# Optimization experiments

Measured on AMD Instinct MI355X. Metric: run time of the kernel, lower is better.

The kernel has to match this reference:

```python
import jax, jax.numpy as jnp
import numpy as np

N = 100000   # nodes
E = 1600000  # edges
F = 64       # node_features == latent_channels
H = 128      # hidden_channels
G = 256      # graphs
L = 2        # n_layers


def setup_inputs() -> dict:
    key = jax.random.key(0)
    ks = jax.random.split(key, 20)
    x = jax.random.normal(ks[0], (N, F), dtype=jnp.float32)
    u = jax.random.normal(ks[1], (G, 2), dtype=jnp.float32)
    edge_index = jax.random.randint(ks[2], (2, E), 0, N, dtype=jnp.int32)
    # evenly assign nodes to graphs (sorted segment ids, no empty segments)
    batch = (jnp.arange(N, dtype=jnp.int32) * G // N).astype(jnp.int32)
    s = 0.05
    # per-layer edge-MLP params, stacked over layers: in = 2F-2 = 126
    W1 = jax.random.normal(ks[3], (L, 2 * F - 2, H), dtype=jnp.float32) * s
    b1 = jnp.zeros((L, H), dtype=jnp.float32)
    W2 = jax.random.normal(ks[4], (L, H, H), dtype=jnp.float32) * s
    b2 = jnp.zeros((L, H), dtype=jnp.float32)
    W3 = jax.random.normal(ks[5], (L, H, F), dtype=jnp.float32) * s
    b3 = jnp.zeros((L, F), dtype=jnp.float32)
    # readout head: in = 3*F + 2 = 194
    LW1 = jax.random.normal(ks[6], (3 * F + 2, F), dtype=jnp.float32) * s
    Lb1 = jnp.zeros((F,), dtype=jnp.float32)
    LW2 = jax.random.normal(ks[7], (F, F), dtype=jnp.float32) * s
    Lb2 = jnp.zeros((F,), dtype=jnp.float32)
    LW3 = jax.random.normal(ks[8], (F, 2), dtype=jnp.float32) * s
    Lb3 = jnp.zeros((2,), dtype=jnp.float32)
    return dict(x=x, u=u, edge_index=edge_index, batch=batch,
                W1=W1, b1=b1, W2=W2, b2=b2, W3=W3, b3=b3,
                LW1=LW1, Lb1=Lb1, LW2=LW2, Lb2=Lb2, LW3=LW3, Lb3=Lb3)


def _edge_layer(x, src, dst, W1, b1, W2, b2, W3, b3):
    xi = x[dst]            # target nodes (x_i), [E, F]
    xj = x[src]            # source nodes (x_j), [E, F]
    d = xj[:, :3] - xi[:, :3]
    dist2 = jnp.sum(d * d, axis=-1, keepdims=True)  # [E, 1]
    m_in = jnp.concatenate([xi, xj[:, 3:], dist2], axis=-1)  # [E, 2F-2]
    h = jax.nn.silu(m_in @ W1 + b1)
    h = jax.nn.silu(h @ W2 + b2)
    m = jax.nn.silu(h @ W3 + b3)                    # [E, F]
    return jax.ops.segment_sum(m, dst, num_segments=N)  # aggr='sum'


def reference(x, u, edge_index, batch, W1, b1, W2, b2, W3, b3,
              LW1, Lb1, LW2, Lb2, LW3, Lb3):
    src, dst = edge_index[0], edge_index[1]
    for l in range(L):
        x = _edge_layer(x, src, dst, W1[l], b1[l], W2[l], b2[l], W3[l], b3[l])
    addp = jax.ops.segment_sum(x, batch, num_segments=G)
    cnt = jax.ops.segment_sum(jnp.ones((N, 1), x.dtype), batch, num_segments=G)
    meanp = addp / jnp.maximum(cnt, 1.0)
    maxp = jax.ops.segment_max(x, batch, num_segments=G)
    pooled = jnp.concatenate([addp, meanp, maxp, u], axis=1)  # [G, 3F+2]
    h = jax.nn.silu(pooled @ LW1 + Lb1)
    h = jax.nn.silu(h @ LW2 + Lb2)
    return h @ LW3 + Lb3  # [G, 2]
```

## Files before the change

### kernel.cpp

```cpp
#include <hip/hip_runtime.h>
#include <hip/hip_bf16.h>

typedef _Float16 f16;
typedef _Float16 f16x8 __attribute__((ext_vector_type(8)));
typedef float    f32x4 __attribute__((ext_vector_type(4)));
typedef float    f32x8 __attribute__((ext_vector_type(8)));

__device__ __forceinline__ float silu_f(float x) {
    return x * __builtin_amdgcn_rcpf(1.0f + __expf(-x));
}

__device__ __forceinline__ f16 exp2h(f16 x) {
    short r, xs = __builtin_bit_cast(short, x);
    asm("v_exp_f16 %0, %1" : "=v"(r) : "v"(xs));
    return __builtin_bit_cast(f16, r);
}
__device__ __forceinline__ f16 rcph(f16 x) {
    short r, xs = __builtin_bit_cast(short, x);
    asm("v_rcp_f16 %0, %1" : "=v"(r) : "v"(xs));
    return __builtin_bit_cast(f16, r);
}
__device__ __forceinline__ f16x8 silu_h8(f16x8 x) {
    f16x8 t = x * (f16)(-1.442695040f);
    f16x8 e;
#pragma unroll
    for (int j = 0; j < 8; j++) e[j] = exp2h(t[j]);
    f16x8 d = e + (f16)1.0f;
    f16x8 r;
#pragma unroll
    for (int j = 0; j < 8; j++) r[j] = rcph(d[j]);
    return x * r;
}

__device__ __forceinline__ void load_lds16(const f16* g, f16* l) {
    __builtin_amdgcn_global_load_lds(
        (const __attribute__((address_space(1))) void*)g,
        (__attribute__((address_space(3))) void*)l, 16, 0, 0);
}

__global__ void prep_kernel(const float* __restrict__ W1, const float* __restrict__ W2,
                            const float* __restrict__ W3, f16* __restrict__ B1T,
                            f16* __restrict__ W2T, f16* __restrict__ W3T,
                            f16* __restrict__ w1c, int L, int total) {
    int idx = blockIdx.x * 256 + threadIdx.x;
    if (idx >= total) return;
    const int per = 16384 + 16384 + 8192 + 128;
    int l = idx / per, r = idx % per;
    const float* W1l = W1 + (size_t)l * 126 * 128;
    if (r < 16384) {
        int c = r >> 6, k = r & 63;
        float v;
        if (c < 128) v = W1l[k * 128 + c];
        else v = (k >= 3) ? W1l[(64 + k - 3) * 128 + (c - 128)] : 0.0f;
        B1T[(size_t)l * 16384 + r] = (f16)v;
    } else if (r < 32768) {
        int q = r - 16384, n = q >> 7, k = q & 127;
        W2T[(size_t)l * 16384 + q] = (f16)W2[(size_t)l * 16384 + k * 128 + n];
    } else if (r < 40960) {
        int q = r - 32768, n = q >> 7, k = q & 127;
        W3T[(size_t)l * 8192 + q] = (f16)W3[(size_t)l * 8192 + k * 64 + n];
    } else {
        int c = r - 40960;
        w1c[l * 128 + c] = (f16)W1l[125 * 128 + c];
    }
}

__global__ void hist_kernel(const int* __restrict__ ei, int* __restrict__ deg, int E) {
    int i = blockIdx.x * 256 + threadIdx.x;
    if (i < E) atomicAdd(&deg[ei[E + i]], 1);
}

__global__ void scan_part(const int* __restrict__ deg, int* __restrict__ bsum, int N) {
    __shared__ int red[256];
    int t = threadIdx.x;
    int i = blockIdx.x * 256 + t;
    red[t] = (i < N) ? deg[i] : 0;
    __syncthreads();
    for (int s = 128; s > 0; s >>= 1) {
        if (t < s) red[t] += red[t + s];
        __syncthreads();
    }
    if (t == 0) bsum[blockIdx.x] = red[0];
}

__global__ void scan_mid(const int* __restrict__ bsum, int* __restrict__ boff, int nb) {
    __shared__ int sm[512];
    int t = threadIdx.x;
    int v = (t < nb) ? bsum[t] : 0;
    sm[t] = v;
    __syncthreads();
    for (int off = 1; off < 512; off <<= 1) {
        int a = (t >= off) ? sm[t - off] : 0;
        __syncthreads();
        sm[t] += a;
        __syncthreads();
    }
    if (t < nb) boff[t] = sm[t] - v;
}

__global__ void scan_final(const int* __restrict__ deg, const int* __restrict__ boff,
                           int* __restrict__ row_start, int N) {
    __shared__ int sm[256];
    int t = threadIdx.x;
    int i = blockIdx.x * 256 + t;
    int v = (i < N) ? deg[i] : 0;
    sm[t] = v;
    __syncthreads();
    for (int off = 1; off < 256; off <<= 1) {
        int a = (t >= off) ? sm[t - off] : 0;
        __syncthreads();
        sm[t] += a;
        __syncthreads();
    }
    if (i < N) row_start[i] = boff[blockIdx.x] + sm[t] - v;
}

__global__ void scatter_kernel(const int* __restrict__ ei, const int* __restrict__ row_start,
                               int* __restrict__ cursor, int2* __restrict__ sd, int E) {
    int i = blockIdx.x * 256 + threadIdx.x;
    if (i < E) {
        int d = ei[E + i];
        int p = row_start[d] + atomicAdd(&cursor[d], 1);
        sd[p] = make_int2(ei[i], d);
    }
}

__global__ __launch_bounds__(256, 3) void node_kernel(
    const float* __restrict__ x, const f16* __restrict__ B1T,
    const float* __restrict__ b1, f16* __restrict__ PQ,
    float4* __restrict__ C, int N, int ntiles) {
    __shared__ f16 b1t[256 * 72];
    const int tid = threadIdx.x;
    const int w = tid >> 6, lane = tid & 63, lm = lane & 15, kg = lane >> 4;

    for (int i = tid; i < 256 * 64; i += 256)
        b1t[(i >> 6) * 72 + (i & 63)] = B1T[i];
    __syncthreads();

    for (int tile = blockIdx.x; tile < ntiles; tile += gridDim.x) {
        const int base = tile * 64;
        int ar = base + w * 16 + lm;
        if (ar >= N) ar = N - 1;

        f16x8 afrag[2];
#pragma unroll
        for (int ks = 0; ks < 2; ks++) {
            f32x8 v = *(const f32x8*)(x + (size_t)ar * 64 + ks * 32 + kg * 8);
            f16x8 h;
#pragma unroll
            for (int j = 0; j < 8; j++) h[j] = (f16)v[j];
            afrag[ks] = h;
        }

        f32x4 acc[16];
#pragma unroll
        for (int nb = 0; nb < 16; nb++) acc[nb] = (f32x4){0.f, 0.f, 0.f, 0.f};
#pragma unroll
        for (int ks = 0; ks < 2; ks++)
#pragma unroll
            for (int nb = 0; nb < 16; nb++) {
                f16x8 b = *(const f16x8*)&b1t[(nb * 16 + lm) * 72 + ks * 32 + kg * 8];
                acc[nb] = __builtin_amdgcn_mfma_f32_16x16x32_f16(afrag[ks], b, acc[nb], 0, 0, 0);
            }

#pragma unroll
        for (int nb = 0; nb < 16; nb++) {
            int col = nb * 16 + lm;
            float bias = (col < 128) ? b1[col] : 0.0f;
#pragma unroll
            for (int reg = 0; reg < 4; reg++) {
                int orow = base + w * 16 + kg * 4 + reg;
                if (orow < N) PQ[(size_t)orow * 256 + col] = (f16)(acc[nb][reg] + bias);
            }
        }
        if (tid < 64) {
            int n = base + tid;
            if (n < N) {
                const float* xr = x + (size_t)n * 64;
                C[n] = make_float4(xr[0], xr[1], xr[2], 0.0f);
            }
        }
    }
}

__global__ __launch_bounds__(256, 3) void edge_kernel(
    const f16* __restrict__ PQ, const float4* __restrict__ C,
    const int2* __restrict__ sd,
    const f16* __restrict__ W2T, const f16* __restrict__ W3T,
    const f16* __restrict__ w1c, const float* __restrict__ b2,
    const float* __restrict__ b3, float* __restrict__ xout,
    int E, int wtiles) {
    __shared__ f16 w2t[128 * 128];
    __shared__ f16 stage[4 * 2048];
    __shared__ f16 tb[4 * 576];

    const int tid = threadIdx.x;
    const int w = tid >> 6, lane = tid & 63, lm = lane & 15, kg = lane >> 4;
    const int e4 = lane >> 2, c4 = lane & 3;

    for (int i = tid; i < 128 * 128; i += 256) {
        int n = i >> 7, k = i & 127;
        w2t[n * 128 + (((k >> 3) ^ (n & 15)) << 3) + (k & 7)] = W2T[i];
    }

    f16x8 wvh[4];
#pragma unroll
    for (int ks = 0; ks < 4; ks++) wvh[ks] = *(const f16x8*)(w1c + ks * 32 + kg * 8);
    float bias2[8], bias3[4];
#pragma unroll
    for (int nb = 0; nb < 8; nb++) bias2[nb] = b2[nb * 16 + lm];
#pragma unroll
    for (int nb = 0; nb < 4; nb++) bias3[nb] = b3[nb * 16 + lm];
    __syncthreads();

    f16* sw = stage + w * 2048;
    f16* tq = tb + w * 576;
    const int nwaves = gridDim.x * 4;
    const int r0 = kg * 4;
    const int l1i = (lane + 16) & 63, l2i = (lane + 32) & 63, l3i = (lane + 48) & 63;

    int t = blockIdx.x * 4 + w;
    if (t >= wtiles) return;
    int e0 = t * 16 + lm;
    int erc = min(e0, E - 1);
    int2 sd0 = sd[erc];
    int scl = sd0.x, dcl = sd0.y;
    int dsen_cur = (e0 < E) ? dcl : -1;
    {
        int se = __shfl(scl, e4);
        const f16* gq = PQ + (size_t)se * 256 + 128 + c4 * 8;
#pragma unroll
        for (int j = 0; j < 4; j++) load_lds16(gq + j * 32, sw + j * 512 + lane * 8);
    }
    f16x8 pv[4];
    {
        const f16* gp = PQ + (size_t)dcl * 256 + kg * 8;
#pragma unroll
        for (int ks = 0; ks < 4; ks++) pv[ks] = *(const f16x8*)(gp + ks * 32);
    }
    int e1 = (t + nwaves) * 16 + lm;
    int erc1 = min(max(e1, 0), E - 1);
    int2 sdn = sd[erc1];
    int s_nx = sdn.x, d_nx = sdn.y;
    int e_nx_ok = (e1 < E) ? 1 : 0;
    float4 cs = C[scl], cd = C[dcl];

    f32x4 acc2p[4];
#pragma unroll
    for (int nb2 = 0; nb2 < 4; nb2++) acc2p[nb2] = (f32x4){0.f, 0.f, 0.f, 0.f};
    int dsen_prev = -1;

    while (true) {
        const int tn = t + nwaves;

        asm volatile("s_waitcnt vmcnt(0)" ::: "memory");

        float dx = cs.x - cd.x, dy = cs.y - cd.y, dz = cs.z - cd.z;
        float dist2 = dx * dx + dy * dy + dz * dz;
        f16 d2h = (f16)dist2;

        f16x8 afrag[4];
#pragma unroll
        for (int ks = 0; ks < 4; ks++) {
            f16x8 q = *(const f16x8*)&sw[ks * 512 + lm * 32 + kg * 8];
            f16x8 xv = pv[ks] + q + d2h * wvh[ks];
            afrag[ks] = silu_h8(xv);
        }

        f32x4 acc1[8];
#pragma unroll
        for (int nb = 0; nb < 8; nb++) acc1[nb] = (f32x4){0.f, 0.f, 0.f, 0.f};
#pragma unroll
        for (int ks = 0; ks < 4; ks++)
#pragma unroll
            for (int nb = 0; nb < 8; nb++) {
                int n = nb * 16 + lm;
                f16x8 b = *(const f16x8*)&w2t[n * 128 + (((ks * 4 + kg) ^ (n & 15)) << 3)];
                acc1[nb] = __builtin_amdgcn_mfma_f32_16x16x32_f16(afrag[ks], b, acc1[nb], 0, 0, 0);
            }

        {
            const int dr0 = __shfl(dsen_prev, r0);
            const int dr1 = __shfl(dsen_prev, r0 + 1);
            const int dr2 = __shfl(dsen_prev, r0 + 2);
            const int dr3 = __shfl(dsen_prev, r0 + 3);
            int prevv = __shfl(dsen_prev, (r0 - 1) & 63);
            if (kg == 0) prevv = -1234567;

            const bool e01 = dr0 == dr1, e12 = dr1 == dr2, e23 = dr2 == dr3;
            const bool c01 = e01, c02 = e01 && e12, c03 = c02 && e23;
            const bool c12 = e12, c13 = e12 && e23;
            const int fullI = c03 ? 1 : 0;

            const int tgt = dr3;
            const int dr0_1 = __shfl(dr0, l1i), fu1 = __shfl(fullI, l1i);
            const int dr0_2 = __shfl(dr0, l2i), fu2 = __shfl(fullI, l2i);
            const int dr0_3 = __shfl(dr0, l3i);
            const bool take1 = (kg <= 2) && (dr0_1 == tgt);
            const bool take2 = take1 && fu1 && (kg <= 1) && (dr0_2 == tgt);
            const bool take3 = take2 && fu2 && (kg == 0) && (dr0_3 == tgt);

            const bool h0 = (dr0 != prevv) && (dr0 >= 0);
            const bool h1f = (!e01) && (dr1 >= 0);
            const bool h2f = (!e12) && (dr2 >= 0);
            const bool h3f = (!e23) && (dr3 >= 0);

            float t0v[4], t1v[4], t2v[4], t3v[4];
#pragma unroll
            for (int nb2 = 0; nb2 < 4; nb2++) {
                const float bias = bias3[nb2];
                const float v0 = silu_f(acc2p[nb2][0] + bias);
                const float v1 = silu_f(acc2p[nb2][1] + bias);
                const float v2 = silu_f(acc2p[nb2][2] + bias);
                const float v3 = silu_f(acc2p[nb2][3] + bias);
                float lead = v0 + (c01 ? v1 : 0.f) + (c02 ? v2 : 0.f) + (c03 ? v3 : 0.f);
                float ext = 0.f;
                const float le1 = __shfl(lead, l1i);
                const float le2 = __shfl(lead, l2i);
                const float le3 = __shfl(lead, l3i);
                if (take1) ext += le1;
                if (take2) ext += le2;
                if (take3) ext += le3;
                t0v[nb2] = lead + (c03 ? ext : 0.f);
                t1v[nb2] = v1 + (c12 ? v2 : 0.f) + (c13 ? (v3 + ext) : 0.f);
                t2v[nb2] = v2 + (e23 ? (v3 + ext) : 0.f);
                t3v[nb2] = v3 + ext;
            }
            if (h0) {
                float* p = xout + (size_t)dr0 * 64 + lm;
#pragma unroll
                for (int nb2 = 0; nb2 < 4; nb2++) atomicAdd(p + nb2 * 16, t0v[nb2]);
            }
            if (h1f) {
                float* p = xout + (size_t)dr1 * 64 + lm;
#pragma unroll
                for (int nb2 = 0; nb2 < 4; nb2++) atomicAdd(p + nb2 * 16, t1v[nb2]);
            }
            if (h2f) {
                float* p = xout + (size_t)dr2 * 64 + lm;
#pragma unroll
                for (int nb2 = 0; nb2 < 4; nb2++) atomicAdd(p + nb2 * 16, t2v[nb2]);
            }
            if (h3f) {
                float* p = xout + (size_t)dr3 * 64 + lm;
#pragma unroll
                for (int nb2 = 0; nb2 < 4; nb2++) atomicAdd(p + nb2 * 16, t3v[nb2]);
            }
        }

        int dsen_nx = e_nx_ok ? d_nx : -1;
        if (tn < wtiles) {
            int se = __shfl(s_nx, e4);
            const f16* gq = PQ + (size_t)se * 256 + 128 + c4 * 8;
#pragma unroll
            for (int j = 0; j < 4; j++) load_lds16(gq + j * 32, sw + j * 512 + lane * 8);
        }

        f16x8 pv2[4];
        {
            const f16* gp2 = PQ + (size_t)d_nx * 256 + kg * 8;
#pragma unroll
            for (int ks = 0; ks < 4; ks++) pv2[ks] = *(const f16x8*)(gp2 + ks * 32);
        }
        int e2 = (tn + nwaves) * 16 + lm;
        int erc2 = min(max(e2, 0), E - 1);
        int2 sd2 = sd[erc2];
        int e_nx2_ok = (e2 < E) ? 1 : 0;
        float4 cs2 = C[s_nx], cd2 = C[d_nx];

        f32x4 acc2[4];
#pragma unroll
        for (int nb2 = 0; nb2 < 4; nb2++) acc2[nb2] = (f32x4){0.f, 0.f, 0.f, 0.f};
#pragma unroll
        for (int kq = 0; kq < 4; kq++) {
#pragma unroll
            for (int nn = 0; nn < 2; nn++) {
                int nb = kq * 2 + nn;
#pragma unroll
                for (int reg = 0; reg < 4; reg++)
                    tq[(kg * 4 + reg) * 36 + nn * 16 + lm] =
                        (f16)silu_f(acc1[nb][reg] + bias2[nb]);
            }
            f16x8 a2 = *(const f16x8*)&tq[lm * 36 + kg * 8];
#pragma unroll
            for (int nb2 = 0; nb2 < 4; nb2++) {
                f16x8 b = *(const f16x8*)(W3T + (size_t)(nb2 * 16 + lm) * 128 +
                                          kq * 32 + kg * 8);
                acc2[nb2] = __builtin_amdgcn_mfma_f32_16x16x32_f16(a2, b, acc2[nb2], 0, 0, 0);
            }
        }

#pragma unroll
        for (int nb2 = 0; nb2 < 4; nb2++) acc2p[nb2] = acc2[nb2];
#pragma unroll
        for (int ks = 0; ks < 4; ks++) pv[ks] = pv2[ks];
        dsen_prev = dsen_cur;
        dsen_cur = dsen_nx;
        s_nx = sd2.x; d_nx = sd2.y; e_nx_ok = e_nx2_ok;
        cs = cs2; cd = cd2;
        t = tn;
        if (t >= wtiles) break;
    }

    {
        const int dr0 = __shfl(dsen_prev, r0);
        const int dr1 = __shfl(dsen_prev, r0 + 1);
        const int dr2 = __shfl(dsen_prev, r0 + 2);
        const int dr3 = __shfl(dsen_prev, r0 + 3);
        int prevv = __shfl(dsen_prev, (r0 - 1) & 63);
        if (kg == 0) prevv = -1234567;

        const bool e01 = dr0 == dr1, e12 = dr1 == dr2, e23 = dr2 == dr3;
        const bool c01 = e01, c02 = e01 && e12, c03 = c02 && e23;
        const bool c12 = e12, c13 = e12 && e23;
        const int fullI = c03 ? 1 : 0;

        const int tgt = dr3;
        const int dr0_1 = __shfl(dr0, l1i), fu1 = __shfl(fullI, l1i);
        const int dr0_2 = __shfl(dr0, l2i), fu2 = __shfl(fullI, l2i);
        const int dr0_3 = __shfl(dr0, l3i);
        const bool take1 = (kg <= 2) && (dr0_1 == tgt);
        const bool take2 = take1 && fu1 && (kg <= 1) && (dr0_2 == tgt);
        const bool take3 = take2 && fu2 && (kg == 0) && (dr0_3 == tgt);

        const bool h0 = (dr0 != prevv) && (dr0 >= 0);
        const bool h1f = (!e01) && (dr1 >= 0);
        const bool h2f = (!e12) && (dr2 >= 0);
        const bool h3f = (!e23) && (dr3 >= 0);

        float t0v[4], t1v[4], t2v[4], t3v[4];
#pragma unroll
        for (int nb2 = 0; nb2 < 4; nb2++) {
            const float bias = bias3[nb2];
            const float v0 = silu_f(acc2p[nb2][0] + bias);
            const float v1 = silu_f(acc2p[nb2][1] + bias);
            const float v2 = silu_f(acc2p[nb2][2] + bias);
            const float v3 = silu_f(acc2p[nb2][3] + bias);
            float lead = v0 + (c01 ? v1 : 0.f) + (c02 ? v2 : 0.f) + (c03 ? v3 : 0.f);
            float ext = 0.f;
            const float le1 = __shfl(lead, l1i);
            const float le2 = __shfl(lead, l2i);
            const float le3 = __shfl(lead, l3i);
            if (take1) ext += le1;
            if (take2) ext += le2;
            if (take3) ext += le3;
            t0v[nb2] = lead + (c03 ? ext : 0.f);
            t1v[nb2] = v1 + (c12 ? v2 : 0.f) + (c13 ? (v3 + ext) : 0.f);
            t2v[nb2] = v2 + (e23 ? (v3 + ext) : 0.f);
            t3v[nb2] = v3 + ext;
        }
        if (h0) {
            float* p = xout + (size_t)dr0 * 64 + lm;
#pragma unroll
            for (int nb2 = 0; nb2 < 4; nb2++) atomicAdd(p + nb2 * 16, t0v[nb2]);
        }
        if (h1f) {
            float* p = xout + (size_t)dr1 * 64 + lm;
#pragma unroll
            for (int nb2 = 0; nb2 < 4; nb2++) atomicAdd(p + nb2 * 16, t1v[nb2]);
        }
        if (h2f) {
            float* p = xout + (size_t)dr2 * 64 + lm;
#pragma unroll
            for (int nb2 = 0; nb2 < 4; nb2++) atomicAdd(p + nb2 * 16, t2v[nb2]);
        }
        if (h3f) {
            float* p = xout + (size_t)dr3 * 64 + lm;
#pragma unroll
            for (int nb2 = 0; nb2 < 4; nb2++) atomicAdd(p + nb2 * 16, t3v[nb2]);
        }
    }
    asm volatile("s_waitcnt vmcnt(0)" ::: "memory");
}

__global__ void pool_head_kernel(const float* __restrict__ xf, const float* __restrict__ u,
                                 const float* __restrict__ LW1, const float* __restrict__ Lb1,
                                 const float* __restrict__ LW2, const float* __restrict__ Lb2,
                                 const float* __restrict__ LW3, const float* __restrict__ Lb3,
                                 float* __restrict__ out, int N, int G) {
    int g = blockIdx.x;
    int t = threadIdx.x;
    int ch = t & 63, sub = t >> 6;
    long long n0 = ((long long)g * N + G - 1) / G;
    long long n1 = ((long long)(g + 1) * N + G - 1) / G;
    float sm = 0.f, mx = -3.0e38f;
    for (long long n = n0 + sub; n < n1; n += 4) {
        float v = xf[n * 64 + ch];
        sm += v;
        mx = fmaxf(mx, v);
    }
    __shared__ float ssum[256], smax[256];
    __shared__ float pl[194];
    __shared__ float hl[64];
    ssum[t] = sm;
    smax[t] = mx;
    __syncthreads();
    if (sub == 0) {
        float a = ssum[ch] + ssum[64 + ch] + ssum[128 + ch] + ssum[192 + ch];
        float m = fmaxf(fmaxf(smax[ch], smax[64 + ch]), fmaxf(smax[128 + ch], smax[192 + ch]));
        float cnt = (float)(n1 - n0);
        pl[ch] = a;
        pl[64 + ch] = a / fmaxf(cnt, 1.f);
        pl[128 + ch] = m;
    }
    if (t == 0) {
        pl[192] = u[g * 2];
        pl[193] = u[g * 2 + 1];
    }
    __syncthreads();
    float a = 0.f;
    if (t < 64) {
        a = Lb1[t];
        for (int k = 0; k < 194; k++) a += pl[k] * LW1[k * 64 + t];
        a = a / (1.0f + __expf(-a));
        hl[t] = a;
    }
    __syncthreads();
    float b = 0.f;
    if (t < 64) {
        b = Lb2[t];
        for (int k = 0; k < 64; k++) b += hl[k] * LW2[k * 64 + t];
        b = b / (1.0f + __expf(-b));
    }
    __syncthreads();
    if (t < 64) hl[t] = b;
    __syncthreads();
    if (t < 2) {
        float c = Lb3[t];
        for (int k = 0; k < 64; k++) c += hl[k] * LW3[k * 2 + t];
        out[g * 2 + t] = c;
    }
}

extern "C" void kernel_launch(void* const* d_in, const int* in_sizes, int n_in,
                              void* d_out, int out_size, void* d_ws, size_t ws_size,
                              hipStream_t stream) {
    const float* x   = (const float*)d_in[0];
    const float* u   = (const float*)d_in[1];
    const int*   ei  = (const int*)d_in[2];
    const float* W1  = (const float*)d_in[4];
    const float* b1  = (const float*)d_in[5];
    const float* W2  = (const float*)d_in[6];
    const float* b2  = (const float*)d_in[7];
    const float* W3  = (const float*)d_in[8];
    const float* b3  = (const float*)d_in[9];
    const float* LW1 = (const float*)d_in[10];
    const float* Lb1 = (const float*)d_in[11];
    const float* LW2 = (const float*)d_in[12];
    const float* Lb2 = (const float*)d_in[13];
    const float* LW3 = (const float*)d_in[14];
    const float* Lb3 = (const float*)d_in[15];

    const int N = in_sizes[0] / 64;
    const int G = in_sizes[1] / 2;
    const int E = in_sizes[2] / 2;
    const int L = in_sizes[4] / (126 * 128);

    char* ws = (char*)d_ws;
    size_t off = 0;
    auto alloc = [&](size_t bytes) -> char* {
        char* p = ws + off;
        off += (bytes + 511) & ~(size_t)511;
        return p;
    };
    f16*    PQ     = (f16*)alloc((size_t)N * 256 * 2);
    float4* C      = (float4*)alloc((size_t)N * 16);
    float*  x1     = (float*)alloc((size_t)N * 64 * 4);
    float*  x2     = (float*)alloc((size_t)N * 64 * 4);
    int2*   sd     = (int2*)alloc((size_t)E * 8);
    int*    deg    = (int*)alloc((size_t)N * 4);
    int*    rowst  = (int*)alloc((size_t)N * 4);
    int*    cursor = (int*)alloc((size_t)N * 4);
    int*    bsum   = (int*)alloc(4096);
    int*    boff   = (int*)alloc(4096);
    f16*    B1T    = (f16*)alloc((size_t)L * 256 * 64 * 2);
    f16*    W2T    = (f16*)alloc((size_t)L * 128 * 128 * 2);
    f16*    W3T    = (f16*)alloc((size_t)L * 64 * 128 * 2);
    f16*    w1c    = (f16*)alloc((size_t)L * 128 * 2);
    (void)ws_size;
    (void)n_in;
    (void)out_size;

    hipMemsetAsync(deg, 0, (size_t)N * 4, stream);
    hipMemsetAsync(cursor, 0, (size_t)N * 4, stream);
    hipMemsetAsync(x1, 0, (size_t)N * 64 * 4, stream);
    hipMemsetAsync(x2, 0, (size_t)N * 64 * 4, stream);

    {
        int total = L * (16384 + 16384 + 8192 + 128);
        prep_kernel<<<(total + 255) / 256, 256, 0, stream>>>(W1, W2, W3, B1T, W2T, W3T, w1c, L, total);
    }
    hist_kernel<<<(E + 255) / 256, 256, 0, stream>>>(ei, deg, E);
    int NB = (N + 255) / 256;
    scan_part<<<NB, 256, 0, stream>>>(deg, bsum, N);
    scan_mid<<<1, 512, 0, stream>>>(bsum, boff, NB);
    scan_final<<<NB, 256, 0, stream>>>(deg, boff, rowst, N);
    scatter_kernel<<<(E + 255) / 256, 256, 0, stream>>>(ei, rowst, cursor, sd, E);

    const float* xcur = x;
    const int wtiles = (E + 15) / 16;
    const int ntiles_node = (N + 63) / 64;
    for (int l = 0; l < L; l++) {
        node_kernel<<<768, 256, 0, stream>>>(xcur, B1T + (size_t)l * 16384, b1 + l * 128,
                                             PQ, C, N, ntiles_node);
        float* xo = (l & 1) ? x2 : x1;
        edge_kernel<<<768, 256, 0, stream>>>(PQ, C, sd,
                                             W2T + (size_t)l * 16384, W3T + (size_t)l * 8192,
                                             w1c + l * 128, b2 + l * 128, b3 + l * 64,
                                             xo, E, wtiles);
        xcur = xo;
    }
    pool_head_kernel<<<G, 256, 0, stream>>>(xcur, u, LW1, Lb1, LW2, Lb2, LW3, Lb3,
                                            (float*)d_out, N, G);
}
```

Baseline: 914.0 us.

## Load source rows into registers, drop LDS staging, raise occupancy to four blocks

```diff
diff --git a/kernel.cpp b/kernel.cpp
--- a/kernel.cpp
+++ b/kernel.cpp
@@ -30,12 +30,6 @@
 #pragma unroll
     for (int j = 0; j < 8; j++) r[j] = rcph(d[j]);
     return x * r;
-}
-
-__device__ __forceinline__ void load_lds16(const f16* g, f16* l) {
-    __builtin_amdgcn_global_load_lds(
-        (const __attribute__((address_space(1))) void*)g,
-        (__attribute__((address_space(3))) void*)l, 16, 0, 0);
 }
 
 __global__ void prep_kernel(const float* __restrict__ W1, const float* __restrict__ W2,
@@ -183,7 +177,7 @@
     }
 }
 
-__global__ __launch_bounds__(256, 3) void edge_kernel(
+__global__ __launch_bounds__(256, 4) void edge_kernel(
     const f16* __restrict__ PQ, const float4* __restrict__ C,
     const int2* __restrict__ sd,
     const f16* __restrict__ W2T, const f16* __restrict__ W3T,
@@ -191,12 +185,10 @@
     const float* __restrict__ b3, float* __restrict__ xout,
     int E, int wtiles) {
     __shared__ f16 w2t[128 * 128];
-    __shared__ f16 stage[4 * 2048];
     __shared__ f16 tb[4 * 576];
 
     const int tid = threadIdx.x;
     const int w = tid >> 6, lane = tid & 63, lm = lane & 15, kg = lane >> 4;
-    const int e4 = lane >> 2, c4 = lane & 3;
 
     for (int i = tid; i < 128 * 128; i += 256) {
         int n = i >> 7, k = i & 127;
@@ -206,14 +198,20 @@
     f16x8 wvh[4];
 #pragma unroll
     for (int ks = 0; ks < 4; ks++) wvh[ks] = *(const f16x8*)(w1c + ks * 32 + kg * 8);
-    float bias2[8], bias3[4];
-#pragma unroll
-    for (int nb = 0; nb < 8; nb++) bias2[nb] = b2[nb * 16 + lm];
+    f16x8 b2v[4];
+#pragma unroll
+    for (int kq = 0; kq < 4; kq++)
+#pragma unroll
+        for (int nn = 0; nn < 2; nn++) {
+            f16 bv = (f16)b2[(kq * 2 + nn) * 16 + lm];
+#pragma unroll
+            for (int reg = 0; reg < 4; reg++) b2v[kq][nn * 4 + reg] = bv;
+        }
+    float bias3[4];
 #pragma unroll
     for (int nb = 0; nb < 4; nb++) bias3[nb] = b3[nb * 16 + lm];
     __syncthreads();
 
-    f16* sw = stage + w * 2048;
     f16* tq = tb + w * 576;
     const int nwaves = gridDim.x * 4;
     const int r0 = kg * 4;
@@ -226,17 +224,15 @@
     int2 sd0 = sd[erc];
     int scl = sd0.x, dcl = sd0.y;
     int dsen_cur = (e0 < E) ? dcl : -1;
-    {
-        int se = __shfl(scl, e4);
-        const f16* gq = PQ + (size_t)se * 256 + 128 + c4 * 8;
-#pragma unroll
-        for (int j = 0; j < 4; j++) load_lds16(gq + j * 32, sw + j * 512 + lane * 8);
-    }
-    f16x8 pv[4];
+    f16x8 pv[4], qv[4];
     {
         const f16* gp = PQ + (size_t)dcl * 256 + kg * 8;
-#pragma unroll
-        for (int ks = 0; ks < 4; ks++) pv[ks] = *(const f16x8*)(gp + ks * 32);
+        const f16* gq = PQ + (size_t)scl * 256 + 128 + kg * 8;
+#pragma unroll
+        for (int ks = 0; ks < 4; ks++) {
+            pv[ks] = *(const f16x8*)(gp + ks * 32);
+            qv[ks] = *(const f16x8*)(gq + ks * 32);
+        }
     }
     int e1 = (t + nwaves) * 16 + lm;
     int erc1 = min(max(e1, 0), E - 1);
@@ -253,8 +249,6 @@
     while (true) {
         const int tn = t + nwaves;
 
-        asm volatile("s_waitcnt vmcnt(0)" ::: "memory");
-
         float dx = cs.x - cd.x, dy = cs.y - cd.y, dz = cs.z - cd.z;
         float dist2 = dx * dx + dy * dy + dz * dz;
         f16 d2h = (f16)dist2;
@@ -262,8 +256,7 @@
         f16x8 afrag[4];
 #pragma unroll
         for (int ks = 0; ks < 4; ks++) {
-            f16x8 q = *(const f16x8*)&sw[ks * 512 + lm * 32 + kg * 8];
-            f16x8 xv = pv[ks] + q + d2h * wvh[ks];
+            f16x8 xv = pv[ks] + qv[ks] + d2h * wvh[ks];
             afrag[ks] = silu_h8(xv);
         }
 
@@ -349,18 +342,15 @@
         }
 
         int dsen_nx = e_nx_ok ? d_nx : -1;
-        if (tn < wtiles) {
-            int se = __shfl(s_nx, e4);
-            const f16* gq = PQ + (size_t)se * 256 + 128 + c4 * 8;
-#pragma unroll
-            for (int j = 0; j < 4; j++) load_lds16(gq + j * 32, sw + j * 512 + lane * 8);
-        }
-
-        f16x8 pv2[4];
+        f16x8 pv2[4], qv2[4];
         {
             const f16* gp2 = PQ + (size_t)d_nx * 256 + kg * 8;
-#pragma unroll
-            for (int ks = 0; ks < 4; ks++) pv2[ks] = *(const f16x8*)(gp2 + ks * 32);
+            const f16* gq2 = PQ + (size_t)s_nx * 256 + 128 + kg * 8;
+#pragma unroll
+            for (int ks = 0; ks < 4; ks++) {
+                pv2[ks] = *(const f16x8*)(gp2 + ks * 32);
+                qv2[ks] = *(const f16x8*)(gq2 + ks * 32);
+            }
         }
         int e2 = (tn + nwaves) * 16 + lm;
         int erc2 = min(max(e2, 0), E - 1);
@@ -373,14 +363,18 @@
         for (int nb2 = 0; nb2 < 4; nb2++) acc2[nb2] = (f32x4){0.f, 0.f, 0.f, 0.f};
 #pragma unroll
         for (int kq = 0; kq < 4; kq++) {
-#pragma unroll
-            for (int nn = 0; nn < 2; nn++) {
-                int nb = kq * 2 + nn;
+            f16x8 hv;
+#pragma unroll
+            for (int nn = 0; nn < 2; nn++)
 #pragma unroll
                 for (int reg = 0; reg < 4; reg++)
-                    tq[(kg * 4 + reg) * 36 + nn * 16 + lm] =
-                        (f16)silu_f(acc1[nb][reg] + bias2[nb]);
-            }
+                    hv[nn * 4 + reg] = (f16)acc1[kq * 2 + nn][reg];
+            hv = silu_h8(hv + b2v[kq]);
+#pragma unroll
+            for (int nn = 0; nn < 2; nn++)
+#pragma unroll
+                for (int reg = 0; reg < 4; reg++)
+                    tq[(kg * 4 + reg) * 36 + nn * 16 + lm] = hv[nn * 4 + reg];
             f16x8 a2 = *(const f16x8*)&tq[lm * 36 + kg * 8];
 #pragma unroll
             for (int nb2 = 0; nb2 < 4; nb2++) {
@@ -393,7 +387,7 @@
 #pragma unroll
         for (int nb2 = 0; nb2 < 4; nb2++) acc2p[nb2] = acc2[nb2];
 #pragma unroll
-        for (int ks = 0; ks < 4; ks++) pv[ks] = pv2[ks];
+        for (int ks = 0; ks < 4; ks++) { pv[ks] = pv2[ks]; qv[ks] = qv2[ks]; }
         dsen_prev = dsen_cur;
         dsen_cur = dsen_nx;
         s_nx = sd2.x; d_nx = sd2.y; e_nx_ok = e_nx2_ok;
@@ -470,7 +464,6 @@
             for (int nb2 = 0; nb2 < 4; nb2++) atomicAdd(p + nb2 * 16, t3v[nb2]);
         }
     }
-    asm volatile("s_waitcnt vmcnt(0)" ::: "memory");
 }
 
 __global__ void pool_head_kernel(const float* __restrict__ xf, const float* __restrict__ u,
@@ -604,10 +597,10 @@
         node_kernel<<<768, 256, 0, stream>>>(xcur, B1T + (size_t)l * 16384, b1 + l * 128,
                                              PQ, C, N, ntiles_node);
         float* xo = (l & 1) ? x2 : x1;
-        edge_kernel<<<768, 256, 0, stream>>>(PQ, C, sd,
-                                             W2T + (size_t)l * 16384, W3T + (size_t)l * 8192,
-                                             w1c + l * 128, b2 + l * 128, b3 + l * 64,
-                                             xo, E, wtiles);
+        edge_kernel<<<1024, 256, 0, stream>>>(PQ, C, sd,
+                                              W2T + (size_t)l * 16384, W3T + (size_t)l * 8192,
+                                              w1c + l * 128, b2 + l * 128, b3 + l * 64,
+                                              xo, E, wtiles);
         xcur = xo;
     }
     pool_head_kernel<<<G, 256, 0, stream>>>(xcur, u, LW1, Lb1, LW2, Lb2, LW3, Lb3,
```

Measured after the change: 1.370 ms. 49.9% more time.
